# Kernel tuning notes

Hardware: AMD Instinct MI355X
Metric: run time of the kernel (lower is better)

The kernel has to match this reference:

```python
import jax, jax.numpy as jnp
import numpy as np

T, A = 2048, 64          # n_thread, n_agents
RAWOB, N_TP, N_GP = 120, 5, 2
E = N_TP * N_GP          # number of sub-nets (type x group placeholder)
D = RAWOB + N_TP + 1     # augmented obs dim fed to each Net
H = 128                  # hidden width of each sub-net MLP
N_ACTION = 16


def setup_inputs() -> dict:
    key = jax.random.key(0)
    ks = jax.random.split(key, 12)
    s1 = 1.0 / np.sqrt(D)
    s2 = 1.0 / np.sqrt(H)
    return {
        "obs": jax.random.normal(ks[0], (T, A, RAWOB), dtype=jnp.float32),
        "hete_pick": jax.random.randint(ks[1], (T, A), 0, E),
        "hete_type": jax.random.randint(ks[2], (T, A), 0, N_TP),
        "gp_sel_summary": jax.random.randint(ks[3], (T, N_TP), 0, N_GP),
        # per-expert actor MLP params [E, ...]
        "W1": jax.random.normal(ks[4], (E, D, H), dtype=jnp.float32) * s1,
        "b1": jnp.zeros((E, H), dtype=jnp.float32),
        "W2": jax.random.normal(ks[5], (E, H, N_ACTION), dtype=jnp.float32) * s2,
        "b2": jnp.zeros((E, N_ACTION), dtype=jnp.float32),
        # central critic params
        "Wc1": jax.random.normal(ks[6], (D, H), dtype=jnp.float32) * s1,
        "bc1": jnp.zeros((H,), dtype=jnp.float32),
        "Wc2": jax.random.normal(ks[7], (H, 1), dtype=jnp.float32) * s2,
        "bc2": jnp.zeros((1,), dtype=jnp.float32),
    }


def _augment_obs(obs, hete_type, gp_sel_summary):
    # obs <- cat(obs, hete_type, gp_sel_summary with -1 scattered at own type idx)
    t, a, _ = obs.shape
    n_tp = gp_sel_summary.shape[1]
    gp = jnp.broadcast_to(gp_sel_summary[:, None, :].astype(obs.dtype), (t, a, n_tp))
    oh = jax.nn.one_hot(hete_type, n_tp, dtype=obs.dtype)
    gp_obs = gp * (1.0 - oh) - oh  # scatter -1 at index hete_type
    return jnp.concatenate([obs, hete_type[..., None].astype(obs.dtype), gp_obs], axis=-1)


def reference(obs, hete_pick, hete_type, gp_sel_summary,
              W1, b1, W2, b2, Wc1, bc1, Wc2, bc2):
    t, a, _ = obs.shape
    x = _augment_obs(obs, hete_type, gp_sel_summary)          # [T, A, D]
    xf = x.reshape(t * a, -1)                                  # [N, D]
    pick = hete_pick.reshape(t * a)                            # [N]
    n_exp = W1.shape[0]
    # dispatch: each token routed to exactly one sub-net; dense compute + masked combine
    logits = jnp.zeros((t * a, W2.shape[-1]), dtype=obs.dtype)
    for e in range(n_exp):  # small fixed expert loop
        y = jax.nn.relu(xf @ W1[e] + b1[e]) @ W2[e] + b2[e]    # [N, n_action]
        logits = jnp.where((pick == e)[:, None], y, logits)
    logits = logits.reshape(t, a, -1)
    # central critic on all tokens
    value = (jax.nn.relu(xf @ Wc1 + bc1) @ Wc2 + bc2).reshape(t, a, 1)
    return logits, value
```

## Files before the change

### kernel.cpp

```cpp
#include <hip/hip_runtime.h>
#include <hip/hip_bf16.h>

#define T_DIM   2048
#define A_DIM   64
#define N_TOK   (T_DIM * A_DIM)
#define RAWOB   120
#define N_TP    5
#define E_EXP   10
#define D_DIM   126
#define DP      128
#define H_DIM   128
#define N_ACT   16
#define CAP     14336
#define BTOK    128
#define MAXC    (CAP / BTOK)
#define LOGITS_SZ (N_TOK * N_ACT)
#define HB_STRIDE 136

typedef __bf16 bh8 __attribute__((ext_vector_type(8)));
typedef ushort u16x8 __attribute__((ext_vector_type(8)));
typedef float  f32x4 __attribute__((ext_vector_type(4)));

__device__ __forceinline__ f32x4 mfma16(bh8 a, bh8 b, f32x4 c) {
    return __builtin_amdgcn_mfma_f32_16x16x32_bf16(a, b, c, 0, 0, 0);
}

__device__ __forceinline__ ushort f2bf(float f) {
    unsigned x = __builtin_bit_cast(unsigned, f);
    unsigned r = (x + 0x7fffu + ((x >> 16) & 1u)) >> 16;
    return (ushort)r;
}

#define W1P_N (E_EXP * H_DIM * DP)
#define W2P_N (E_EXP * N_ACT * H_DIM)
#define WC1P_N (DP * DP)
#define PREP_BLOCKS 124

__global__ __launch_bounds__(256) void prep_kernel(
    const float* __restrict__ W1, const float* __restrict__ W2,
    const float* __restrict__ Wc1,
    int* __restrict__ counts, ushort* __restrict__ W1p,
    ushort* __restrict__ W2p, ushort* __restrict__ Wc1p)
{
    int bx = blockIdx.x, tid = threadIdx.x;
    if (bx < 44) {
        __shared__ ushort st[32][130];
        const float* src;
        ushort* dstbase;
        int kt;
        if (bx < 40) {
            int e = bx >> 2;
            kt = bx & 3;
            src = W1 + (e * D_DIM + kt * 32) * H_DIM;
            dstbase = W1p + e * (H_DIM * DP);
        } else {
            kt = bx - 40;
            src = Wc1 + kt * 32 * H_DIM;
            dstbase = Wc1p;
        }
        int dmax = D_DIM - kt * 32;
#pragma unroll
        for (int p = 0; p < 16; ++p) {
            int idx = p * 256 + tid;
            int dd = idx >> 7, n = idx & 127;
            float v = (dd < dmax) ? src[dd * H_DIM + n] : 0.f;
            st[dd][n] = f2bf(v);
        }
        __syncthreads();
#pragma unroll
        for (int p = 0; p < 16; ++p) {
            int idx = p * 256 + tid;
            int dd = idx >> 7, n = idx & 127;
            dstbase[((n >> 4) * 4 + kt) * 512 + ((dd >> 3) * 16 + (n & 15)) * 8 + (dd & 7)]
                = st[dd][n];
        }
    } else {
        int i = (bx - 44) * 256 + tid;
        int j = i & 7;
        int l = (i >> 3) & 63;
        int kt = (i >> 9) & 3;
        int e = i >> 11;
        int lm = l & 15, lq = l >> 4;
        W2p[i] = f2bf(W2[(e * H_DIM + kt * 32 + lq * 8 + j) * N_ACT + lm]);
        if (bx == 44 && tid < 160) counts[tid] = 0;
    }
}

#define BUCKET_BLOCKS 128
__global__ __launch_bounds__(256) void bucket_kernel(
    const int* __restrict__ pick, int* __restrict__ counts, int* __restrict__ order)
{
    __shared__ int lc[E_EXP], lb[E_EXP], lcur[E_EXP];
    int tid = threadIdx.x;
    if (tid < E_EXP) { lc[tid] = 0; lcur[tid] = 0; }
    __syncthreads();
    int base = blockIdx.x * 1024;
    int e4[4];
#pragma unroll
    for (int it = 0; it < 4; ++it) {
        e4[it] = pick[base + it * 256 + tid];
        atomicAdd(&lc[e4[it]], 1);
    }
    __syncthreads();
    if (tid < E_EXP) lb[tid] = atomicAdd(&counts[tid * 16], lc[tid]);
    __syncthreads();
#pragma unroll
    for (int it = 0; it < 4; ++it) {
        int e = e4[it];
        int pos = lb[e] + atomicAdd(&lcur[e], 1);
        if (pos < CAP) order[e * CAP + pos] = base + it * 256 + tid;
    }
}

__global__ __launch_bounds__(256, 5) void moe_kernel(
    const float* __restrict__ obs, const int* __restrict__ hete_type,
    const int* __restrict__ gp_sel,
    const float* __restrict__ b1, const float* __restrict__ b2,
    const float* __restrict__ bc1, const float* __restrict__ bc2,
    const int* __restrict__ counts, const int* __restrict__ order,
    const ushort* __restrict__ W1p, const ushort* __restrict__ W2p,
    const ushort* __restrict__ Wc1p, const float* __restrict__ Wc2,
    float* __restrict__ out)
{
    __shared__ __align__(16) ushort hbuf[4][32 * HB_STRIDE];

    const int bx = blockIdx.x;
    const int e = bx % E_EXP;
    const int c = bx / E_EXP;
    const int cnt = counts[e * 16];
    const int tid = threadIdx.x;
    const int w = tid >> 6;
    const int base = c * BTOK + w * 32;
    if (base >= cnt) return;

    const int l = tid & 63;
    const int lm = l & 15;
    const int lq = l >> 4;

    const int* ord_e = order + e * CAP;

    bh8 a[2][4];
#pragma unroll
    for (int mt = 0; mt < 2; ++mt) {
        const int slot = min(base + mt * 16 + lm, cnt - 1);
        const int tok = ord_e[slot];
        const float* orow = obs + tok * RAWOB;
#pragma unroll
        for (int kt = 0; kt < 3; ++kt) {
            const float* p = orow + kt * 32 + lq * 8;
            float4 u0 = *(const float4*)(const void*)p;
            float4 u1 = *(const float4*)(const void*)(p + 4);
            u16x8 t;
            t[0] = f2bf(u0.x); t[1] = f2bf(u0.y); t[2] = f2bf(u0.z); t[3] = f2bf(u0.w);
            t[4] = f2bf(u1.x); t[5] = f2bf(u1.y); t[6] = f2bf(u1.z); t[7] = f2bf(u1.w);
            a[mt][kt] = __builtin_bit_cast(bh8, t);
        }
        u16x8 t;
        if (lq < 3) {
            const float* p = orow + 96 + lq * 8;
            float4 u0 = *(const float4*)(const void*)p;
            float4 u1 = *(const float4*)(const void*)(p + 4);
            t[0] = f2bf(u0.x); t[1] = f2bf(u0.y); t[2] = f2bf(u0.z); t[3] = f2bf(u0.w);
            t[4] = f2bf(u1.x); t[5] = f2bf(u1.y); t[6] = f2bf(u1.z); t[7] = f2bf(u1.w);
        } else {
            int ht = hete_type[tok];
            int tt = tok >> 6;
            t[0] = f2bf((float)ht);
#pragma unroll
            for (int q = 0; q < N_TP; ++q) {
                float g = (q == ht) ? -1.0f : (float)gp_sel[tt * N_TP + q];
                t[1 + q] = f2bf(g);
            }
            t[6] = 0; t[7] = 0;
        }
        a[mt][3] = __builtin_bit_cast(bh8, t);
    }

    ushort* hrow = &hbuf[w][0];
    const ushort* W1e = W1p + e * (H_DIM * DP);
    float part[2][4] = {{0.f,0.f,0.f,0.f},{0.f,0.f,0.f,0.f}};
#pragma unroll
    for (int nt = 0; nt < 8; ++nt) {
        const int n = nt * 16 + lm;
        f32x4 ae0 = (f32x4){0.f,0.f,0.f,0.f}, ae1 = ae0, ac0 = ae0, ac1 = ae0;
#pragma unroll
        for (int kt = 0; kt < 4; ++kt) {
            bh8 be = *(const bh8*)(const void*)(W1e + (nt * 4 + kt) * 512 + l * 8);
            bh8 bc = *(const bh8*)(const void*)(Wc1p + (nt * 4 + kt) * 512 + l * 8);
            ae0 = mfma16(a[0][kt], be, ae0);
            ae1 = mfma16(a[1][kt], be, ae1);
            ac0 = mfma16(a[0][kt], bc, ac0);
            ac1 = mfma16(a[1][kt], bc, ac1);
        }
        float bn = b1[e * H_DIM + n];
        float cn = bc1[n];
        float wc = Wc2[n];
#pragma unroll
        for (int r = 0; r < 4; ++r) {
            hrow[(lq * 4 + r) * HB_STRIDE + n] = f2bf(fmaxf(ae0[r] + bn, 0.f));
            hrow[(16 + lq * 4 + r) * HB_STRIDE + n] = f2bf(fmaxf(ae1[r] + bn, 0.f));
            part[0][r] += fmaxf(ac0[r] + cn, 0.f) * wc;
            part[1][r] += fmaxf(ac1[r] + cn, 0.f) * wc;
        }
    }

#pragma unroll
    for (int mask = 1; mask < 16; mask <<= 1)
#pragma unroll
        for (int mt = 0; mt < 2; ++mt)
#pragma unroll
            for (int r = 0; r < 4; ++r)
                part[mt][r] += __shfl_xor(part[mt][r], mask, 64);
    if (lm == 0) {
        float bcv = bc2[0];
#pragma unroll
        for (int mt = 0; mt < 2; ++mt)
#pragma unroll
            for (int r = 0; r < 4; ++r) {
                int m = mt * 16 + lq * 4 + r;
                if (base + m < cnt)
                    out[LOGITS_SZ + ord_e[base + m]] = part[mt][r] + bcv;
            }
    }

    {
        f32x4 y0 = (f32x4){0.f,0.f,0.f,0.f}, y1 = y0;
#pragma unroll
        for (int kt = 0; kt < 4; ++kt) {
            bh8 bf = *(const bh8*)(const void*)(W2p + (e * 4 + kt) * 512 + l * 8);
            bh8 h0 = *(const bh8*)(const void*)(hrow + lm * HB_STRIDE + kt * 32 + lq * 8);
            bh8 h1 = *(const bh8*)(const void*)(hrow + (16 + lm) * HB_STRIDE + kt * 32 + lq * 8);
            y0 = mfma16(h0, bf, y0);
            y1 = mfma16(h1, bf, y1);
        }
        float bb = b2[e * N_ACT + lm];
#pragma unroll
        for (int r = 0; r < 4; ++r) {
            int m0 = lq * 4 + r;
            if (base + m0 < cnt)
                out[ord_e[base + m0] * N_ACT + lm] = y0[r] + bb;
            int m1 = 16 + lq * 4 + r;
            if (base + m1 < cnt)
                out[ord_e[base + m1] * N_ACT + lm] = y1[r] + bb;
        }
    }
}

extern "C" void kernel_launch(void* const* d_in, const int* in_sizes, int n_in,
                              void* d_out, int out_size, void* d_ws, size_t ws_size,
                              hipStream_t stream) {
    const float* obs  = (const float*)d_in[0];
    const int*   pick = (const int*)d_in[1];
    const int*   htyp = (const int*)d_in[2];
    const int*   gp   = (const int*)d_in[3];
    const float* W1   = (const float*)d_in[4];
    const float* b1   = (const float*)d_in[5];
    const float* W2   = (const float*)d_in[6];
    const float* b2   = (const float*)d_in[7];
    const float* Wc1  = (const float*)d_in[8];
    const float* bc1  = (const float*)d_in[9];
    const float* Wc2  = (const float*)d_in[10];
    const float* bc2  = (const float*)d_in[11];
    float* out = (float*)d_out;

    int*    counts = (int*)d_ws;
    int*    order  = counts + 160;
    ushort* W1p    = (ushort*)(order + E_EXP * CAP);
    ushort* W2p    = W1p + W1P_N;
    ushort* Wc1p   = W2p + W2P_N;

    prep_kernel<<<PREP_BLOCKS, 256, 0, stream>>>(
        W1, W2, Wc1, counts, W1p, W2p, Wc1p);
    bucket_kernel<<<BUCKET_BLOCKS, 256, 0, stream>>>(pick, counts, order);
    moe_kernel<<<E_EXP * MAXC, 256, 0, stream>>>(
        obs, htyp, gp, b1, b2, bc1, bc2, counts, order,
        W1p, W2p, Wc1p, Wc2, out);
}
```

Measured before the change: 150.7 us.

## Stage expert and critic weights in LDS and split expert/critic phases

Each block cooperatively copies its expert's W1 and W2 into shared memory, runs the expert MLP from LDS, then overwrites the buffer with the critic Wc1 and computes the critic value in a second phase. Bias and critic-scale values are hoisted into registers before the loops. The goal is to replace repeated per-wave global/L2 weight fetches with LDS reads and to lower live accumulators by separating the two GEMMs. In exchange it adds block-wide barriers and about 36 KB of extra LDS per block, and lowers the launch-bounds occupancy hint from 5 to 2.

```diff
diff --git a/kernel.cpp b/kernel.cpp
--- a/kernel.cpp
+++ b/kernel.cpp
@@ -112,7 +112,7 @@
     }
 }
 
-__global__ __launch_bounds__(256, 5) void moe_kernel(
+__global__ __launch_bounds__(256, 2) void moe_kernel(
     const float* __restrict__ obs, const int* __restrict__ hete_type,
     const int* __restrict__ gp_sel,
     const float* __restrict__ b1, const float* __restrict__ b2,
@@ -122,20 +122,31 @@
     const ushort* __restrict__ Wc1p, const float* __restrict__ Wc2,
     float* __restrict__ out)
 {
+    __shared__ __align__(16) ushort wlds[18432];
     __shared__ __align__(16) ushort hbuf[4][32 * HB_STRIDE];
 
     const int bx = blockIdx.x;
     const int e = bx % E_EXP;
     const int c = bx / E_EXP;
     const int cnt = counts[e * 16];
+    const int start = c * BTOK;
+    if (start >= cnt) return;
+
     const int tid = threadIdx.x;
     const int w = tid >> 6;
-    const int base = c * BTOK + w * 32;
-    if (base >= cnt) return;
-
+    const int base = start + w * 32;
     const int l = tid & 63;
     const int lm = l & 15;
     const int lq = l >> 4;
+
+    {
+        const u16x8* s1 = (const u16x8*)(const void*)(W1p + e * (H_DIM * DP));
+        u16x8* d1 = (u16x8*)(void*)wlds;
+#pragma unroll
+        for (int p = 0; p < 8; ++p) d1[p * 256 + tid] = s1[p * 256 + tid];
+        ((u16x8*)(void*)(wlds + 16384))[tid] =
+            ((const u16x8*)(const void*)(W2p + e * 2048))[tid];
+    }
 
     const int* ord_e = order + e * CAP;
 
@@ -176,64 +187,48 @@
         a[mt][3] = __builtin_bit_cast(bh8, t);
     }
 
+    float bnv[8], cnv[8], wcv[8];
+#pragma unroll
+    for (int nt = 0; nt < 8; ++nt) {
+        int n = nt * 16 + lm;
+        bnv[nt] = b1[e * H_DIM + n];
+        cnv[nt] = bc1[n];
+        wcv[nt] = Wc2[n];
+    }
+    const float bb  = b2[e * N_ACT + lm];
+    const float bcv = bc2[0];
+
+    __syncthreads();
+
     ushort* hrow = &hbuf[w][0];
-    const ushort* W1e = W1p + e * (H_DIM * DP);
-    float part[2][4] = {{0.f,0.f,0.f,0.f},{0.f,0.f,0.f,0.f}};
 #pragma unroll
     for (int nt = 0; nt < 8; ++nt) {
         const int n = nt * 16 + lm;
-        f32x4 ae0 = (f32x4){0.f,0.f,0.f,0.f}, ae1 = ae0, ac0 = ae0, ac1 = ae0;
+        f32x4 ae0 = (f32x4){0.f,0.f,0.f,0.f}, ae1 = ae0;
 #pragma unroll
         for (int kt = 0; kt < 4; ++kt) {
-            bh8 be = *(const bh8*)(const void*)(W1e + (nt * 4 + kt) * 512 + l * 8);
-            bh8 bc = *(const bh8*)(const void*)(Wc1p + (nt * 4 + kt) * 512 + l * 8);
+            bh8 be = *(const bh8*)(const void*)(wlds + (nt * 4 + kt) * 512 + l * 8);
             ae0 = mfma16(a[0][kt], be, ae0);
             ae1 = mfma16(a[1][kt], be, ae1);
-            ac0 = mfma16(a[0][kt], bc, ac0);
-            ac1 = mfma16(a[1][kt], bc, ac1);
-        }
-        float bn = b1[e * H_DIM + n];
-        float cn = bc1[n];
-        float wc = Wc2[n];
+        }
+        float bn = bnv[nt];
 #pragma unroll
         for (int r = 0; r < 4; ++r) {
             hrow[(lq * 4 + r) * HB_STRIDE + n] = f2bf(fmaxf(ae0[r] + bn, 0.f));
             hrow[(16 + lq * 4 + r) * HB_STRIDE + n] = f2bf(fmaxf(ae1[r] + bn, 0.f));
-            part[0][r] += fmaxf(ac0[r] + cn, 0.f) * wc;
-            part[1][r] += fmaxf(ac1[r] + cn, 0.f) * wc;
-        }
-    }
-
-#pragma unroll
-    for (int mask = 1; mask < 16; mask <<= 1)
-#pragma unroll
-        for (int mt = 0; mt < 2; ++mt)
-#pragma unroll
-            for (int r = 0; r < 4; ++r)
-                part[mt][r] += __shfl_xor(part[mt][r], mask, 64);
-    if (lm == 0) {
-        float bcv = bc2[0];
-#pragma unroll
-        for (int mt = 0; mt < 2; ++mt)
-#pragma unroll
-            for (int r = 0; r < 4; ++r) {
-                int m = mt * 16 + lq * 4 + r;
-                if (base + m < cnt)
-                    out[LOGITS_SZ + ord_e[base + m]] = part[mt][r] + bcv;
-            }
+        }
     }
 
     {
         f32x4 y0 = (f32x4){0.f,0.f,0.f,0.f}, y1 = y0;
 #pragma unroll
         for (int kt = 0; kt < 4; ++kt) {
-            bh8 bf = *(const bh8*)(const void*)(W2p + (e * 4 + kt) * 512 + l * 8);
+            bh8 bf = *(const bh8*)(const void*)(wlds + 16384 + kt * 512 + l * 8);
             bh8 h0 = *(const bh8*)(const void*)(hrow + lm * HB_STRIDE + kt * 32 + lq * 8);
             bh8 h1 = *(const bh8*)(const void*)(hrow + (16 + lm) * HB_STRIDE + kt * 32 + lq * 8);
             y0 = mfma16(h0, bf, y0);
             y1 = mfma16(h1, bf, y1);
         }
-        float bb = b2[e * N_ACT + lm];
 #pragma unroll
         for (int r = 0; r < 4; ++r) {
             int m0 = lq * 4 + r;
@@ -242,6 +237,53 @@
             int m1 = 16 + lq * 4 + r;
             if (base + m1 < cnt)
                 out[ord_e[base + m1] * N_ACT + lm] = y1[r] + bb;
+        }
+    }
+
+    __syncthreads();
+
+    {
+        const u16x8* s1 = (const u16x8*)(const void*)Wc1p;
+        u16x8* d1 = (u16x8*)(void*)wlds;
+#pragma unroll
+        for (int p = 0; p < 8; ++p) d1[p * 256 + tid] = s1[p * 256 + tid];
+    }
+    __syncthreads();
+
+    {
+        float part[2][4] = {{0.f,0.f,0.f,0.f},{0.f,0.f,0.f,0.f}};
+#pragma unroll
+        for (int nt = 0; nt < 8; ++nt) {
+            f32x4 ac0 = (f32x4){0.f,0.f,0.f,0.f}, ac1 = ac0;
+#pragma unroll
+            for (int kt = 0; kt < 4; ++kt) {
+                bh8 bc = *(const bh8*)(const void*)(wlds + (nt * 4 + kt) * 512 + l * 8);
+                ac0 = mfma16(a[0][kt], bc, ac0);
+                ac1 = mfma16(a[1][kt], bc, ac1);
+            }
+            float cn = cnv[nt], wc = wcv[nt];
+#pragma unroll
+            for (int r = 0; r < 4; ++r) {
+                part[0][r] += fmaxf(ac0[r] + cn, 0.f) * wc;
+                part[1][r] += fmaxf(ac1[r] + cn, 0.f) * wc;
+            }
+        }
+#pragma unroll
+        for (int mask = 1; mask < 16; mask <<= 1)
+#pragma unroll
+            for (int mt = 0; mt < 2; ++mt)
+#pragma unroll
+                for (int r = 0; r < 4; ++r)
+                    part[mt][r] += __shfl_xor(part[mt][r], mask, 64);
+        if (lm == 0) {
+#pragma unroll
+            for (int mt = 0; mt < 2; ++mt)
+#pragma unroll
+                for (int r = 0; r < 4; ++r) {
+                    int m = mt * 16 + lq * 4 + r;
+                    if (base + m < cnt)
+                        out[LOGITS_SZ + ord_e[base + m]] = part[mt][r] + bcv;
+                }
         }
     }
 }
```

Result: no change. 148.1 us (-1.7%).
